# Optimization experiments

Hardware: AMD Instinct MI355X
Metric: run time of the kernel (lower is better)

Reference implementation:

```python
import jax, jax.numpy as jnp
import numpy as np

N_EVENT = 100000
N_TRACE = 20000
E_EE = 1000000
E_ET = 500000
E_TE = 500000
D = 128          # embedding_dim == hidden_dim
OUT = 64         # output_dim
L = 3            # num_layers
NTYPES_EDGES = 3 # edge types
B = 64           # graphs per batch


def setup_inputs() -> dict:
    key = jax.random.key(0)
    ks = jax.random.split(key, 16)
    s = 1.0 / np.sqrt(D)
    inp = {
        "event_ids": jnp.arange(N_EVENT, dtype=jnp.int64 if jax.config.jax_enable_x64 else jnp.int32),
        "trace_ids": jnp.arange(N_TRACE, dtype=jnp.int64 if jax.config.jax_enable_x64 else jnp.int32),
        "e2e_src": jax.random.randint(ks[0], (E_EE,), 0, N_EVENT),
        "e2e_dst": jax.random.randint(ks[1], (E_EE,), 0, N_EVENT),
        "e2t_src": jax.random.randint(ks[2], (E_ET,), 0, N_EVENT),
        "e2t_dst": jax.random.randint(ks[3], (E_ET,), 0, N_TRACE),
        "t2e_src": jax.random.randint(ks[4], (E_TE,), 0, N_TRACE),
        "t2e_dst": jax.random.randint(ks[5], (E_TE,), 0, N_EVENT),
        "event_batch": jnp.sort(jax.random.randint(ks[6], (N_EVENT,), 0, B)),
        "trace_batch": jnp.sort(jax.random.randint(ks[7], (N_TRACE,), 0, B)),
        # learned parameters
        "emb_event": jax.random.normal(ks[8], (N_EVENT, D), jnp.float32),
        "emb_trace": jax.random.normal(ks[9], (N_TRACE, D), jnp.float32),
        # per-layer, per-edge-type SAGEConv weights: lin_l (neighbor, with bias), lin_r (root, no bias)
        "Wl": jax.random.normal(ks[10], (L, NTYPES_EDGES, D, D), jnp.float32) * s,
        "bl": jnp.zeros((L, NTYPES_EDGES, D), jnp.float32),
        "Wr": jax.random.normal(ks[11], (L, NTYPES_EDGES, D, D), jnp.float32) * s,
        # output MLP head
        "W1": jax.random.normal(ks[12], (D, D), jnp.float32) * s,
        "b1": jnp.zeros((D,), jnp.float32),
        "W2": jax.random.normal(ks[13], (OUT, D), jnp.float32) * s,
        "b2": jnp.zeros((OUT,), jnp.float32),
    }
    return inp


def reference(event_ids, trace_ids, e2e_src, e2e_dst, e2t_src, e2t_dst,
              t2e_src, t2e_dst, event_batch, trace_batch,
              emb_event, emb_trace, Wl, bl, Wr, W1, b1, W2, b2):
    def seg_mean(x_src, src, dst, n_dst):
        # mean-aggregate source features onto destination nodes (SAGEConv default aggr)
        s = jax.ops.segment_sum(x_src[src], dst, num_segments=n_dst)
        c = jax.ops.segment_sum(jnp.ones(dst.shape, x_src.dtype), dst, num_segments=n_dst)
        return s / jnp.maximum(c, 1.0)[:, None]

    # per-node-type embedding lookup
    x = {"event": emb_event[event_ids], "trace": emb_trace[trace_ids]}
    n = {"event": event_ids.shape[0], "trace": trace_ids.shape[0]}
    # edge types: (src_type, dst_type, src_idx, dst_idx), conv index matches Wl/bl/Wr axis 1
    edges = [
        ("event", "event", e2e_src, e2e_dst),
        ("event", "trace", e2t_src, e2t_dst),
        ("trace", "event", t2e_src, t2e_dst),
    ]
    n_layers = Wl.shape[0]
    for l in range(n_layers):
        new = {k: jnp.zeros((n[k], Wl.shape[-2]), x[k].dtype) for k in x}
        for i, (st, dt, s_idx, d_idx) in enumerate(edges):
            m = seg_mean(x[st], s_idx, d_idx, n[dt])
            # SAGEConv: lin_l(mean neighbors) + lin_r(root); HeteroConv aggr='sum' across edge types
            new[dt] = new[dt] + m @ Wl[l, i].T + bl[l, i] + x[dt] @ Wr[l, i].T
        x = new
    # global_add_pool per node type, then stack+sum over node types
    pooled = (jax.ops.segment_sum(x["event"], event_batch, num_segments=B)
              + jax.ops.segment_sum(x["trace"], trace_batch, num_segments=B))
    h = jax.nn.relu(pooled @ W1.T + b1)
    return h @ W2.T + b2
```

## Files before the change

kernel.cpp:

```cpp
#include <hip/hip_runtime.h>
#include <hip/hip_bf16.h>


#define D 128
#define NB 64
#define OUTD 64
#define NLAY 3
#define EPB 4096
#define BSH2 9
#define PSPLIT 4

typedef __bf16 bf16;
typedef __bf16 bf16x4 __attribute__((ext_vector_type(4)));
typedef __bf16 bf16x8 __attribute__((ext_vector_type(8)));
typedef float  f32x16 __attribute__((ext_vector_type(16)));

#define LOAD16_TO_LDS(gp, lp) \
    __builtin_amdgcn_global_load_lds((const __attribute__((address_space(1))) void*)(gp), \
                                     (__attribute__((address_space(3))) void*)(lp), 16, 0, 0)

__device__ __forceinline__ void pool_block_dev(const bf16* __restrict__ x, int s,
                                               const int* __restrict__ bounds, int b, int j,
                                               float* __restrict__ pooled5, float red[16][D]) {
    int start = bounds[b], end = bounds[b + 1];
    int len = end - start;
    if (len <= 0) return;
    int r0 = start + (int)(((long long)len * j) / PSPLIT);
    int r1 = start + (int)(((long long)len * (j + 1)) / PSPLIT);
    if (r0 >= r1) return;
    int slot = threadIdx.x >> 4;
    int ch   = threadIdx.x & 15;
    float a[8] = {};
    for (int r = r0 + slot; r < r1; r += 16) {
        bf16x8 v = ((const bf16x8*)(x + (size_t)r * D))[ch];
        #pragma unroll
        for (int e = 0; e < 8; ++e) a[e] += (float)v[e];
    }
    #pragma unroll
    for (int e = 0; e < 8; ++e) red[slot][ch * 8 + e] = a[e];
    __syncthreads();
    int c = threadIdx.x;
    if (c < D) {
        float ssum = 0.f;
        #pragma unroll
        for (int k = 0; k < 16; ++k) ssum += red[k][c];
        atomicAdd(&pooled5[(size_t)s * NB * D + b * D + c], ssum);
    }
}

__global__ void front_all(const float* __restrict__ embE, const int* __restrict__ idsE,
                          bf16* __restrict__ xE, int nE,
                          const float* __restrict__ embT, const int* __restrict__ idsT,
                          bf16* __restrict__ xT, int nT,
                          const int* __restrict__ bEv, const int* __restrict__ bTr,
                          int* __restrict__ boundsE, int* __restrict__ boundsT,
                          const int* __restrict__ dEE, int nEE, int nbkEE, int nblkEE,
                          int* __restrict__ cntEE,
                          const int* __restrict__ dET, int nET, int nbkET, int nblkET,
                          int* __restrict__ cntET,
                          const int* __restrict__ dTE, int nTE, int nbkTE, int nblkTE,
                          int* __restrict__ cntTE,
                          const float* __restrict__ Wl, const float* __restrict__ Wr,
                          const float* __restrict__ bl,
                          bf16* __restrict__ wbuf, float* __restrict__ bbuf,
                          float* __restrict__ pooled5, int nGather) {
    __shared__ int h[256];
    int b = blockIdx.x;
    if (b < nGather) {
        int idx = b * 256 + threadIdx.x;
        const float* emb; const int* ids; bf16* x;
        int tE = nE * 32;
        if (idx < tE) { emb = embE; ids = idsE; x = xE; }
        else {
            idx -= tE;
            if (idx >= nT * 32) return;
            emb = embT; ids = idsT; x = xT;
        }
        int r = idx >> 5, v = idx & 31;
        float4 f = ((const float4*)(emb + (size_t)ids[r] * D))[v];
        bf16x4 o;
        o[0] = (bf16)f.x; o[1] = (bf16)f.y; o[2] = (bf16)f.z; o[3] = (bf16)f.w;
        ((bf16x4*)(x + (size_t)r * D))[v] = o;
        return;
    }
    b -= nGather;
    int nblkH = nblkEE + nblkET + nblkTE;
    if (b < nblkH) {
        const int* dst; int E, nbk, nblk, lb; int* cnt;
        if (b < nblkEE) { dst = dEE; E = nEE; nbk = nbkEE; nblk = nblkEE; cnt = cntEE; lb = b; }
        else if (b < nblkEE + nblkET) { dst = dET; E = nET; nbk = nbkET; nblk = nblkET; cnt = cntET; lb = b - nblkEE; }
        else { dst = dTE; E = nTE; nbk = nbkTE; nblk = nblkTE; cnt = cntTE; lb = b - nblkEE - nblkET; }
        h[threadIdx.x] = 0;
        __syncthreads();
        int e0 = lb * EPB, e1 = min(e0 + EPB, E);
        for (int e = e0 + threadIdx.x; e < e1; e += 256) atomicAdd(&h[dst[e] >> BSH2], 1);
        __syncthreads();
        for (int k = threadIdx.x; k < nbk; k += 256) cnt[k * nblk + lb] = h[k];
        return;
    }
    b -= nblkH;
    if (b < 120) {
        int idx = b * 256 + threadIdx.x;
        if (idx >= NLAY * 5 * 2048) return;
        int l = idx / (5 * 2048);
        int rem = idx - l * 5 * 2048;
        int mat = rem >> 11;
        int q = rem & 2047;
        int lane = q & 63, t = (q >> 6) & 7, w = q >> 9;
        int r = w * 32 + (lane & 31);
        int c = t * 16 + (lane >> 5) * 8;
        size_t l3 = (size_t)l * 3;
        const float* s0;
        const float* s1 = nullptr;
        switch (mat) {
            case 0: s0 = Wl + (l3 + 0) * D * D; break;
            case 1: s0 = Wl + (l3 + 2) * D * D; break;
            case 2: s0 = Wr + (l3 + 0) * D * D; s1 = Wr + (l3 + 2) * D * D; break;
            case 3: s0 = Wl + (l3 + 1) * D * D; break;
            default: s0 = Wr + (l3 + 1) * D * D; break;
        }
        bf16x8 hi, lo;
        #pragma unroll
        for (int e = 0; e < 8; ++e) {
            float v = s0[r * D + c + e];
            if (s1) v += s1[r * D + c + e];
            bf16 hh = (bf16)v;
            hi[e] = hh;
            lo[e] = (bf16)(v - (float)hh);
        }
        bf16* base = wbuf + (size_t)l * 10 * D * D;
        ((bf16x8*)(base + (size_t)(2 * mat) * D * D))[q] = hi;
        ((bf16x8*)(base + (size_t)(2 * mat + 1) * D * D))[q] = lo;
        return;
    }
    b -= 120;
    if (b < 2) {
        int idx = b * 256 + threadIdx.x;
        if (idx >= NLAY * D) return;
        int l = idx >> 7, o = idx & (D - 1);
        bbuf[l * 2 * D + o]     = bl[(size_t)(l * 3 + 0) * D + o] + bl[(size_t)(l * 3 + 2) * D + o];
        bbuf[l * 2 * D + D + o] = bl[(size_t)(l * 3 + 1) * D + o];
        return;
    }
    b -= 2;
    if (b == 0) {
        int t = threadIdx.x;
        if (t <= NB) {
            int lo = 0, hi = nE;
            while (lo < hi) { int mid = (lo + hi) >> 1; if (bEv[mid] < t) lo = mid + 1; else hi = mid; }
            boundsE[t] = lo;
        } else if (t <= 2 * NB + 1) {
            int v = t - NB - 1;
            int lo = 0, hi = nT;
            while (lo < hi) { int mid = (lo + hi) >> 1; if (bTr[mid] < v) lo = mid + 1; else hi = mid; }
            boundsT[v] = lo;
        }
        return;
    }
    b -= 1;
    int idx = b * 256 + threadIdx.x;
    if (idx < 5 * NB * D / 4)
        ((float4*)pooled5)[idx] = make_float4(0.f, 0.f, 0.f, 0.f);
}

__global__ void scan_p1_all(const int* __restrict__ dA, int* __restrict__ oA, int* __restrict__ sA, int nA,
                            const int* __restrict__ dB, int* __restrict__ oB, int* __restrict__ sB, int nB,
                            const int* __restrict__ dC, int* __restrict__ oC, int* __restrict__ sC, int nC) {
    int nbA = (nA + 1023) >> 10, nbB = (nB + 1023) >> 10;
    int b = blockIdx.x;
    const int* deg; int* off; int* bsum; int n; int lb;
    if (b < nbA) { deg = dA; off = oA; bsum = sA; n = nA; lb = b; }
    else if (b < nbA + nbB) { deg = dB; off = oB; bsum = sB; n = nB; lb = b - nbA; }
    else { deg = dC; off = oC; bsum = sC; n = nC; lb = b - nbA - nbB; }
    __shared__ int s[256];
    int t = threadIdx.x;
    int base = lb * 1024 + t * 4;
    int v[4];
    #pragma unroll
    for (int i = 0; i < 4; ++i) v[i] = (base + i < n) ? deg[base + i] : 0;
    int tot = v[0] + v[1] + v[2] + v[3];
    s[t] = tot;
    __syncthreads();
    for (int st = 1; st < 256; st <<= 1) {
        int x = (t >= st) ? s[t - st] : 0;
        __syncthreads();
        s[t] += x;
        __syncthreads();
    }
    int run = s[t] - tot;
    #pragma unroll
    for (int i = 0; i < 4; ++i) {
        if (base + i < n) off[base + i] = run;
        run += v[i];
    }
    if (t == 255) bsum[lb] = s[255];
}

__global__ void scan_p23_all(int* __restrict__ oA, const int* __restrict__ sA, int nA,
                             int* __restrict__ oB, const int* __restrict__ sB, int nB,
                             int* __restrict__ oC, const int* __restrict__ sC, int nC) {
    int cbA = (nA + 255) >> 8, cbB = (nB + 255) >> 8;
    int b = blockIdx.x;
    int* off; const int* bsum; int n; int lb;
    if (b < cbA) { off = oA; bsum = sA; n = nA; lb = b; }
    else if (b < cbA + cbB) { off = oB; bsum = sB; n = nB; lb = b - cbA; }
    else { off = oC; bsum = sC; n = nC; lb = b - cbA - cbB; }
    __shared__ int s[256];
    __shared__ int ex[256];
    int nb = (n + 1023) >> 10;
    int t = threadIdx.x;
    int v = (t < nb) ? bsum[t] : 0;
    s[t] = v;
    __syncthreads();
    for (int st = 1; st < 256; st <<= 1) {
        int x = (t >= st) ? s[t - st] : 0;
        __syncthreads();
        s[t] += x;
        __syncthreads();
    }
    ex[t] = s[t] - v;
    __syncthreads();
    int i = lb * 256 + t;
    if (i < n) off[i] += ex[i >> 10];
    if (i == 0) off[n] = s[nb - 1];
}

__global__ void bkt_scatter_all(const int* __restrict__ sEE, const int* __restrict__ dEE,
                                int nEE, int nbkEE, int nblkEE, const int* __restrict__ SEE,
                                int2* __restrict__ ebEE,
                                const int* __restrict__ sET, const int* __restrict__ dET,
                                int nET, int nbkET, int nblkET, const int* __restrict__ SET,
                                int2* __restrict__ ebET,
                                const int* __restrict__ sTE, const int* __restrict__ dTE,
                                int nTE, int nbkTE, int nblkTE, const int* __restrict__ STE,
                                int2* __restrict__ ebTE) {
    __shared__ int cu[256];
    int b = blockIdx.x;
    const int* src; const int* dst; const int* S; int2* eb; int E, nbk, nblk, lb;
    if (b < nblkEE) { src = sEE; dst = dEE; S = SEE; eb = ebEE; E = nEE; nbk = nbkEE; nblk = nblkEE; lb = b; }
    else if (b < nblkEE + nblkET) { src = sET; dst = dET; S = SET; eb = ebET; E = nET; nbk = nbkET; nblk = nblkET; lb = b - nblkEE; }
    else { src = sTE; dst = dTE; S = STE; eb = ebTE; E = nTE; nbk = nbkTE; nblk = nblkTE; lb = b - nblkEE - nblkET; }
    for (int k = threadIdx.x; k < nbk; k += 256) cu[k] = S[k * nblk + lb];
    __syncthreads();
    int e0 = lb * EPB, e1 = min(e0 + EPB, E);
    for (int e = e0 + threadIdx.x; e < e1; e += 256) {
        int s = src[e], d = dst[e];
        int p = atomicAdd(&cu[d >> BSH2], 1);
        eb[p] = make_int2(s, d);
    }
}

__global__ void csr_build_all(const int2* __restrict__ ebEE, const int* __restrict__ SEE,
                              int nbkEE, int nblkEE, int ndEE,
                              int* __restrict__ offEE, int* __restrict__ adjEE,
                              const int2* __restrict__ ebET, const int* __restrict__ SET,
                              int nbkET, int nblkET, int ndET,
                              int* __restrict__ offET, int* __restrict__ adjET,
                              const int2* __restrict__ ebTE, const int* __restrict__ STE,
                              int nbkTE, int nblkTE, int ndTE,
                              int* __restrict__ offTE, int* __restrict__ adjTE) {
    __shared__ int h[512];
    __shared__ int ps[256];
    __shared__ int cc[512];
    int b = blockIdx.x;
    const int2* eb; const int* S; int nbk, nblk, ndst, k; int* off; int* adj;
    if (b < nbkEE) { eb = ebEE; S = SEE; nbk = nbkEE; nblk = nblkEE; ndst = ndEE; off = offEE; adj = adjEE; k = b; }
    else if (b < nbkEE + nbkET) { eb = ebET; S = SET; nbk = nbkET; nblk = nblkET; ndst = ndET; off = offET; adj = adjET; k = b - nbkEE; }
    else { eb = ebTE; S = STE; nbk = nbkTE; nblk = nblkTE; ndst = ndTE; off = offTE; adj = adjTE; k = b - nbkEE - nbkET; }
    int base = S[k * nblk];
    int end  = (k == nbk - 1) ? S[nbk * nblk] : S[(k + 1) * nblk];
    int d0 = k << BSH2;
    int t = threadIdx.x;
    h[t] = 0; h[t + 256] = 0;
    __syncthreads();
    for (int j = base + t; j < end; j += 256) atomicAdd(&h[eb[j].y - d0], 1);
    __syncthreads();
    int a0 = h[2 * t], a1 = h[2 * t + 1];
    ps[t] = a0 + a1;
    __syncthreads();
    for (int st = 1; st < 256; st <<= 1) {
        int x = (t >= st) ? ps[t - st] : 0;
        __syncthreads();
        ps[t] += x;
        __syncthreads();
    }
    int pe = ps[t] - (a0 + a1);
    int o0 = base + pe, o1 = base + pe + a0;
    cc[2 * t] = o0; cc[2 * t + 1] = o1;
    int nd = min(512, ndst - d0);
    if (2 * t < nd) off[d0 + 2 * t] = o0;
    if (2 * t + 1 < nd) off[d0 + 2 * t + 1] = o1;
    if (t == 0 && k == nbk - 1) off[ndst] = end;
    __syncthreads();
    for (int j = base + t; j < end; j += 256) {
        int2 e = eb[j];
        int p = atomicAdd(&cc[e.y - d0], 1);
        adj[p] = e.x;
    }
}

__global__ void agg_all(const bf16* __restrict__ xE, const bf16* __restrict__ xT,
                        const int* __restrict__ offEE, const int* __restrict__ adjEE,
                        const int* __restrict__ offTE, const int* __restrict__ adjTE,
                        const int* __restrict__ offET, const int* __restrict__ adjET,
                        bf16* __restrict__ mEE, bf16* __restrict__ mTE, bf16* __restrict__ mET,
                        int nE, int nT, int aggBlocks,
                        const int* __restrict__ boundsE, const int* __restrict__ boundsT,
                        float* __restrict__ pooled5) {
    __shared__ float red[16][D];
    if ((int)blockIdx.x >= aggBlocks) {
        int idx = (int)blockIdx.x - aggBlocks;
        int j2 = idx / (NB * PSPLIT);
        int rem = idx - j2 * NB * PSPLIT;
        int bb = rem / PSPLIT, jj = rem - bb * PSPLIT;
        if (j2 == 0) pool_block_dev(xE, 2, boundsE, bb, jj, pooled5, red);
        else         pool_block_dev(xT, 4, boundsT, bb, jj, pooled5, red);
        return;
    }
    int gw = (blockIdx.x * blockDim.x + threadIdx.x) >> 6;
    int lane = threadIdx.x & 63;
    int qE = (nE + 3) >> 2, qT = (nT + 3) >> 2;
    const bf16* xsrc; const int* off; const int* adj; bf16* out; int ndst;
    if (gw < qE) { xsrc = xE; off = offEE; adj = adjEE; out = mEE; ndst = nE; }
    else if (gw < 2 * qE) { gw -= qE; xsrc = xT; off = offTE; adj = adjTE; out = mTE; ndst = nE; }
    else {
        gw -= 2 * qE;
        if (gw >= qT) return;
        xsrc = xE; off = offET; adj = adjET; out = mET; ndst = nT;
    }
    int sub = lane >> 4;
    int sl  = lane & 15;
    int row = gw * 4 + sub;
    if (row >= ndst) row = ndst - 1;
    int s0 = off[row], s1 = off[row + 1];
    float a[8] = {};
    int j = s0;
    for (; j + 8 <= s1; j += 8) {
        int ii[8];
        #pragma unroll
        for (int u = 0; u < 8; ++u) ii[u] = adj[j + u];
        bf16x8 v[8];
        #pragma unroll
        for (int u = 0; u < 8; ++u) v[u] = ((const bf16x8*)(xsrc + (size_t)ii[u] * D))[sl];
        #pragma unroll
        for (int u = 0; u < 8; ++u)
            #pragma unroll
            for (int e = 0; e < 8; ++e) a[e] += (float)v[u][e];
    }
    for (; j + 4 <= s1; j += 4) {
        int i0 = adj[j], i1 = adj[j + 1], i2 = adj[j + 2], i3 = adj[j + 3];
        bf16x8 v0 = ((const bf16x8*)(xsrc + (size_t)i0 * D))[sl];
        bf16x8 v1 = ((const bf16x8*)(xsrc + (size_t)i1 * D))[sl];
        bf16x8 v2 = ((const bf16x8*)(xsrc + (size_t)i2 * D))[sl];
        bf16x8 v3 = ((const bf16x8*)(xsrc + (size_t)i3 * D))[sl];
        #pragma unroll
        for (int e = 0; e < 8; ++e)
            a[e] += (float)v0[e] + (float)v1[e] + (float)v2[e] + (float)v3[e];
    }
    for (; j < s1; ++j) {
        int i0 = adj[j];
        bf16x8 v0 = ((const bf16x8*)(xsrc + (size_t)i0 * D))[sl];
        #pragma unroll
        for (int e = 0; e < 8; ++e) a[e] += (float)v0[e];
    }
    float inv = 1.0f / fmaxf((float)(s1 - s0), 1.0f);
    bf16x8 o;
    #pragma unroll
    for (int e = 0; e < 8; ++e) o[e] = (bf16)(a[e] * inv);
    ((bf16x8*)(out + (size_t)row * D))[sl] = o;
}

__device__ __forceinline__ void gemm_body(const bf16* A0, const bf16* A1, const bf16* A2,
                                          const bf16* Wp, const float* bias, bf16* out,
                                          int M, int nm, int row0, bf16* As) {
    int tid = threadIdx.x;
    int wave = tid >> 6, lane = tid & 63;
    int m = lane & 31, half = lane >> 5;

    f32x16 acc[2];
    #pragma unroll
    for (int rt = 0; rt < 2; ++rt)
        #pragma unroll
        for (int i = 0; i < 16; ++i) acc[rt][i] = 0.f;

    const bf16* Aptr[3] = {A0, A1, A2};
    #pragma unroll
    for (int s = 0; s < 3; ++s) {
        if (s >= nm) break;
        if (s) __syncthreads();
        const bf16* Amat = Aptr[s];
        #pragma unroll
        for (int p = 0; p < 4; ++p) {
            int si = p * 256 + tid;
            int r = si >> 4, u = si & 15;
            int gr = row0 + r; if (gr >= M) gr = M - 1;
            int gc = (u ^ (r & 15)) * 8;
            LOAD16_TO_LDS(Amat + (size_t)gr * D + gc, As + (size_t)(p * 4 + wave) * 512);
        }
        const bf16* wph = Wp + (size_t)(2 * s) * D * D + ((size_t)wave * 512 + lane) * 8;
        const bf16* wpl = wph + D * D;
        bf16x8 bh_c  = *(const bf16x8*)(wph);
        bf16x8 blo_c = *(const bf16x8*)(wpl);
        __syncthreads();

        #pragma unroll 1
        for (int t = 0; t < 8; ++t) {
            bf16x8 bh_n, blo_n;
            if (t < 7) {
                bh_n  = *(const bf16x8*)(wph + (t + 1) * 512);
                blo_n = *(const bf16x8*)(wpl + (t + 1) * 512);
            }
            bf16x8 af[2];
            #pragma unroll
            for (int rt = 0; rt < 2; ++rt) {
                int r = rt * 32 + m;
                int c = t * 2 + half;
                af[rt] = *(const bf16x8*)(As + ((size_t)r * 16 + (c ^ (r & 15))) * 8);
            }
            acc[0] = __builtin_amdgcn_mfma_f32_32x32x16_bf16(af[0], bh_c,  acc[0], 0, 0, 0);
            acc[1] = __builtin_amdgcn_mfma_f32_32x32x16_bf16(af[1], bh_c,  acc[1], 0, 0, 0);
            acc[0] = __builtin_amdgcn_mfma_f32_32x32x16_bf16(af[0], blo_c, acc[0], 0, 0, 0);
            acc[1] = __builtin_amdgcn_mfma_f32_32x32x16_bf16(af[1], blo_c, acc[1], 0, 0, 0);
            bh_c = bh_n; blo_c = blo_n;
        }
    }

    int col = wave * 32 + m;
    float bv = bias[col];
    #pragma unroll
    for (int rt = 0; rt < 2; ++rt) {
        #pragma unroll
        for (int r = 0; r < 16; ++r) {
            int row = row0 + rt * 32 + (r & 3) + 8 * (r >> 2) + 4 * half;
            if (row < M) out[(size_t)row * D + col] = (bf16)(acc[rt][r] + bv);
        }
    }
}

__global__ __launch_bounds__(256) void gemm_all(const bf16* __restrict__ eA0, const bf16* __restrict__ eA1,
                                                const bf16* __restrict__ eA2, const bf16* __restrict__ eW,
                                                const float* __restrict__ eB, bf16* __restrict__ eOut,
                                                int Me, int bE,
                                                const bf16* __restrict__ tA0, const bf16* __restrict__ tA1,
                                                const bf16* __restrict__ tW, const float* __restrict__ tB,
                                                bf16* __restrict__ tOut, int Mt) {
    __shared__ bf16 As[64 * 128];
    if ((int)blockIdx.x < bE)
        gemm_body(eA0, eA1, eA2, eW, eB, eOut, Me, 3, blockIdx.x * 64, As);
    else
        gemm_body(tA0, tA1, (const bf16*)nullptr, tW, tB, tOut, Mt, 2,
                  ((int)blockIdx.x - bE) * 64, As);
}

__global__ void pool_m_all(const bf16* __restrict__ m_ee, const bf16* __restrict__ m_te,
                           const bf16* __restrict__ m_et,
                           const int* __restrict__ boundsE, const int* __restrict__ boundsT,
                           float* __restrict__ pooled5) {
    __shared__ float red[16][D];
    int blk = blockIdx.x;
    int s3 = blk / (NB * PSPLIT);
    int rem = blk - s3 * NB * PSPLIT;
    int b = rem / PSPLIT, j = rem - b * PSPLIT;
    if (s3 == 0)      pool_block_dev(m_ee, 0, boundsE, b, j, pooled5, red);
    else if (s3 == 1) pool_block_dev(m_te, 1, boundsE, b, j, pooled5, red);
    else              pool_block_dev(m_et, 3, boundsT, b, j, pooled5, red);
}

__global__ void tail_kernel(const float* __restrict__ pooled5,
                            const int* __restrict__ boundsE, const int* __restrict__ boundsT,
                            const float* __restrict__ Wl, const float* __restrict__ Wr,
                            const float* __restrict__ bl,
                            const float* __restrict__ W1, const float* __restrict__ b1,
                            const float* __restrict__ W2, const float* __restrict__ b2,
                            float* __restrict__ out) {
    __shared__ float p5[5][D];
    __shared__ float hp[D];
    __shared__ float hh[D];
    int b = blockIdx.x, t = threadIdx.x;
    #pragma unroll
    for (int s = 0; s < 5; ++s) p5[s][t] = pooled5[(size_t)(s * NB + b) * D + t];
    __syncthreads();
    float ce = (float)(boundsE[b + 1] - boundsE[b]);
    float ct = (float)(boundsT[b + 1] - boundsT[b]);
    float s = ce * (bl[6 * D + t] + bl[8 * D + t]) + ct * bl[7 * D + t];
    const float* w0  = Wl + (size_t)6 * D * D + (size_t)t * D;
    const float* w2  = Wl + (size_t)8 * D * D + (size_t)t * D;
    const float* wr0 = Wr + (size_t)6 * D * D + (size_t)t * D;
    const float* wr2 = Wr + (size_t)8 * D * D + (size_t)t * D;
    const float* w1m = Wl + (size_t)7 * D * D + (size_t)t * D;
    const float* wr1 = Wr + (size_t)7 * D * D + (size_t)t * D;
    #pragma unroll 4
    for (int k = 0; k < D; ++k)
        s += p5[0][k] * w0[k] + p5[1][k] * w2[k] + p5[2][k] * (wr0[k] + wr2[k])
           + p5[3][k] * w1m[k] + p5[4][k] * wr1[k];
    hp[t] = s;
    __syncthreads();
    float s1 = b1[t];
    const float* u = W1 + (size_t)t * D;
    #pragma unroll 4
    for (int k = 0; k < D; ++k) s1 += hp[k] * u[k];
    hh[t] = fmaxf(s1, 0.f);
    __syncthreads();
    if (t < OUTD) {
        float s2 = b2[t];
        const float* v = W2 + (size_t)t * D;
        #pragma unroll 4
        for (int k = 0; k < D; ++k) s2 += hh[k] * v[k];
        out[b * OUTD + t] = s2;
    }
}

extern "C" void kernel_launch(void* const* d_in, const int* in_sizes, int n_in,
                              void* d_out, int out_size, void* d_ws, size_t ws_size,
                              hipStream_t stream) {
    const int* event_ids   = (const int*)d_in[0];
    const int* trace_ids   = (const int*)d_in[1];
    const int* e2e_src     = (const int*)d_in[2];
    const int* e2e_dst     = (const int*)d_in[3];
    const int* e2t_src     = (const int*)d_in[4];
    const int* e2t_dst     = (const int*)d_in[5];
    const int* t2e_src     = (const int*)d_in[6];
    const int* t2e_dst     = (const int*)d_in[7];
    const int* event_batch = (const int*)d_in[8];
    const int* trace_batch = (const int*)d_in[9];
    const float* emb_event = (const float*)d_in[10];
    const float* emb_trace = (const float*)d_in[11];
    const float* Wl        = (const float*)d_in[12];
    const float* bl        = (const float*)d_in[13];
    const float* Wr        = (const float*)d_in[14];
    const float* W1        = (const float*)d_in[15];
    const float* b1        = (const float*)d_in[16];
    const float* W2        = (const float*)d_in[17];
    const float* b2        = (const float*)d_in[18];

    const int NE = in_sizes[0];
    const int NT = in_sizes[1];
    const int EE = in_sizes[2];
    const int ET = in_sizes[4];
    const int TE = in_sizes[6];

    const int nbkEE = (NE + 511) >> BSH2, nblkEE = (EE + EPB - 1) / EPB;
    const int nbkET = (NT + 511) >> BSH2, nblkET = (ET + EPB - 1) / EPB;
    const int nbkTE = (NE + 511) >> BSH2, nblkTE = (TE + EPB - 1) / EPB;
    const int cEE = nbkEE * nblkEE, cET = nbkET * nblkET, cTE = nbkTE * nblkTE;

    size_t cur = 0;
    auto alloc = [&](size_t bytes) -> void* {
        cur = (cur + 255) & ~(size_t)255;
        void* p = (char*)d_ws + cur;
        cur += bytes;
        return p;
    };
    bf16* x_event   = (bf16*)alloc((size_t)NE * D * 2);
    bf16* x_trace   = (bf16*)alloc((size_t)NT * D * 2);
    bf16* nx_event  = (bf16*)alloc((size_t)NE * D * 2);
    bf16* nx_trace  = (bf16*)alloc((size_t)NT * D * 2);
    bf16* m_ee      = (bf16*)alloc((size_t)NE * D * 2);
    bf16* m_te      = (bf16*)alloc((size_t)NE * D * 2);
    bf16* m_et      = (bf16*)alloc((size_t)NT * D * 2);
    bf16* wbuf      = (bf16*)alloc((size_t)NLAY * 10 * D * D * 2);
    float* bbuf     = (float*)alloc((size_t)NLAY * 2 * D * 4);
    float* pooled5  = (float*)alloc((size_t)5 * NB * D * 4);
    int* boundsE = (int*)alloc((size_t)(NB + 1) * 4);
    int* boundsT = (int*)alloc((size_t)(NB + 1) * 4);
    int* off_ee = (int*)alloc((size_t)(NE + 1) * 4);
    int* adj_ee = (int*)alloc((size_t)EE * 4);
    int* off_et = (int*)alloc((size_t)(NT + 1) * 4);
    int* adj_et = (int*)alloc((size_t)ET * 4);
    int* off_te = (int*)alloc((size_t)(NE + 1) * 4);
    int* adj_te = (int*)alloc((size_t)TE * 4);
    int* cnt_ee = (int*)alloc((size_t)cEE * 4);
    int* S_ee   = (int*)alloc((size_t)(cEE + 1) * 4);
    int* cnt_et = (int*)alloc((size_t)cET * 4);
    int* S_et   = (int*)alloc((size_t)(cET + 1) * 4);
    int* cnt_te = (int*)alloc((size_t)cTE * 4);
    int* S_te   = (int*)alloc((size_t)(cTE + 1) * 4);
    int* bsum_ee = (int*)alloc(((size_t)(cEE + 1023) / 1024 + 1) * 4);
    int* bsum_et = (int*)alloc(((size_t)(cET + 1023) / 1024 + 1) * 4);
    int* bsum_te = (int*)alloc(((size_t)(cTE + 1023) / 1024 + 1) * 4);
    int2* eb_ee = (int2*)m_ee;
    int2* eb_et = (int2*)m_te;
    int2* eb_te = (int2*)m_et;
    (void)ws_size; (void)n_in; (void)out_size;

    const int nGather = ((NE + NT) * 32 + 255) / 256;
    const int nblkH = nblkEE + nblkET + nblkTE;
    front_all<<<nGather + nblkH + 120 + 2 + 1 + 40, 256, 0, stream>>>(
        emb_event, event_ids, x_event, NE, emb_trace, trace_ids, x_trace, NT,
        event_batch, trace_batch, boundsE, boundsT,
        e2e_dst, EE, nbkEE, nblkEE, cnt_ee,
        e2t_dst, ET, nbkET, nblkET, cnt_et,
        t2e_dst, TE, nbkTE, nblkTE, cnt_te,
        Wl, Wr, bl, wbuf, bbuf, pooled5, nGather);

    const int nb1 = (cEE + 1023) >> 10, nb2 = (cET + 1023) >> 10, nb3 = (cTE + 1023) >> 10;
    scan_p1_all<<<nb1 + nb2 + nb3, 256, 0, stream>>>(
        cnt_ee, S_ee, bsum_ee, cEE, cnt_et, S_et, bsum_et, cET, cnt_te, S_te, bsum_te, cTE);
    scan_p23_all<<<((cEE + 255) >> 8) + ((cET + 255) >> 8) + ((cTE + 255) >> 8), 256, 0, stream>>>(
        S_ee, bsum_ee, cEE, S_et, bsum_et, cET, S_te, bsum_te, cTE);
    bkt_scatter_all<<<nblkEE + nblkET + nblkTE, 256, 0, stream>>>(
        e2e_src, e2e_dst, EE, nbkEE, nblkEE, S_ee, eb_ee,
        e2t_src, e2t_dst, ET, nbkET, nblkET, S_et, eb_et,
        t2e_src, t2e_dst, TE, nbkTE, nblkTE, S_te, eb_te);
    csr_build_all<<<nbkEE + nbkET + nbkTE, 256, 0, stream>>>(
        eb_ee, S_ee, nbkEE, nblkEE, NE, off_ee, adj_ee,
        eb_et, S_et, nbkET, nblkET, NT, off_et, adj_et,
        eb_te, S_te, nbkTE, nblkTE, NE, off_te, adj_te);

    const int qE = (NE + 3) >> 2, qT = (NT + 3) >> 2;
    const int aggBlocks = (2 * qE + qT + 3) / 4;
    const int bE = (NE + 63) / 64, bT = (NT + 63) / 64;
    for (int l = 0; l < NLAY; ++l) {
        int extra = (l == NLAY - 1) ? 2 * NB * PSPLIT : 0;
        agg_all<<<aggBlocks + extra, 256, 0, stream>>>(x_event, x_trace,
                                                       off_ee, adj_ee, off_te, adj_te, off_et, adj_et,
                                                       m_ee, m_te, m_et, NE, NT, aggBlocks,
                                                       boundsE, boundsT, pooled5);
        if (l < NLAY - 1) {
            const bf16* wl_ev = wbuf + (size_t)l * 10 * D * D;
            const bf16* wl_tr = wl_ev + (size_t)6 * D * D;
            const float* be = bbuf + (size_t)l * 2 * D;
            const float* bt = be + D;
            gemm_all<<<bE + bT, 256, 0, stream>>>(m_ee, m_te, x_event, wl_ev, be, nx_event, NE, bE,
                                                  m_et, x_trace, wl_tr, bt, nx_trace, NT);
            bf16* t;
            t = x_event; x_event = nx_event; nx_event = t;
            t = x_trace; x_trace = nx_trace; nx_trace = t;
        }
    }

    pool_m_all<<<3 * NB * PSPLIT, 256, 0, stream>>>(m_ee, m_te, m_et,
                                                    boundsE, boundsT, pooled5);
    tail_kernel<<<NB, D, 0, stream>>>(pooled5, boundsE, boundsT, Wl, Wr, bl,
                                      W1, b1, W2, b2, (float*)d_out);
}
```

Baseline: 561.2 us.

## Merge CSR build phases and pooling tail into cooperative kernels with grid sync

Four CSR construction kernels (scan phase 1, scan phase 2/3, bucket scatter, CSR build) become one cooperative kernel that separates the phases with grid-wide syncs. The pooling and MLP-tail kernels are likewise merged into a second cooperative kernel. The aim is to cut kernel launch overhead and inter-kernel gaps. In exchange, each phase runs on a fixed grid of 512 blocks with grid.sync barriers, which can add barrier cost and reduce parallelism for phases that used more blocks.

```diff
diff --git a/kernel.cpp b/kernel.cpp
--- a/kernel.cpp
+++ b/kernel.cpp
@@ -1,5 +1,8 @@
 #include <hip/hip_runtime.h>
 #include <hip/hip_bf16.h>
+#include <hip/hip_cooperative_groups.h>
+
+namespace cg = cooperative_groups;
 
 
 #define D 128
@@ -9,6 +12,8 @@
 #define EPB 4096
 #define BSH2 9
 #define PSPLIT 4
+#define CSRGRID 512
+#define FINGRID 512
 
 typedef __bf16 bf16;
 typedef __bf16 bf16x4 __attribute__((ext_vector_type(4)));
@@ -46,6 +51,7 @@
         for (int k = 0; k < 16; ++k) ssum += red[k][c];
         atomicAdd(&pooled5[(size_t)s * NB * D + b * D + c], ssum);
     }
+    __syncthreads();
 }
 
 __global__ void front_all(const float* __restrict__ embE, const int* __restrict__ idsE,
@@ -163,16 +169,25 @@
         ((float4*)pooled5)[idx] = make_float4(0.f, 0.f, 0.f, 0.f);
 }
 
-__global__ void scan_p1_all(const int* __restrict__ dA, int* __restrict__ oA, int* __restrict__ sA, int nA,
-                            const int* __restrict__ dB, int* __restrict__ oB, int* __restrict__ sB, int nB,
-                            const int* __restrict__ dC, int* __restrict__ oC, int* __restrict__ sC, int nC) {
-    int nbA = (nA + 1023) >> 10, nbB = (nB + 1023) >> 10;
-    int b = blockIdx.x;
+struct CsrArgs {
+    const int *sEE, *dEE, *sET, *dET, *sTE, *dTE;
+    int nEE, nET, nTE;
+    int nbkEE, nblkEE, nbkET, nblkET, nbkTE, nblkTE;
+    int cEE, cET, cTE;
+    int *cnt_ee, *S_ee, *cnt_et, *S_et, *cnt_te, *S_te;
+    int *bsum_ee, *bsum_et, *bsum_te;
+    int2 *eb_ee, *eb_et, *eb_te;
+    int *off_ee, *adj_ee, *off_et, *adj_et, *off_te, *adj_te;
+    int ndEE, ndET, ndTE;
+};
+
+__device__ void scan_p1_dev(int b, const CsrArgs& A, int* sh) {
+    int nbA = (A.cEE + 1023) >> 10, nbB = (A.cET + 1023) >> 10;
     const int* deg; int* off; int* bsum; int n; int lb;
-    if (b < nbA) { deg = dA; off = oA; bsum = sA; n = nA; lb = b; }
-    else if (b < nbA + nbB) { deg = dB; off = oB; bsum = sB; n = nB; lb = b - nbA; }
-    else { deg = dC; off = oC; bsum = sC; n = nC; lb = b - nbA - nbB; }
-    __shared__ int s[256];
+    if (b < nbA) { deg = A.cnt_ee; off = A.S_ee; bsum = A.bsum_ee; n = A.cEE; lb = b; }
+    else if (b < nbA + nbB) { deg = A.cnt_et; off = A.S_et; bsum = A.bsum_et; n = A.cET; lb = b - nbA; }
+    else { deg = A.cnt_te; off = A.S_te; bsum = A.bsum_te; n = A.cTE; lb = b - nbA - nbB; }
+    int* s = sh;
     int t = threadIdx.x;
     int base = lb * 1024 + t * 4;
     int v[4];
@@ -194,19 +209,17 @@
         run += v[i];
     }
     if (t == 255) bsum[lb] = s[255];
-}
-
-__global__ void scan_p23_all(int* __restrict__ oA, const int* __restrict__ sA, int nA,
-                             int* __restrict__ oB, const int* __restrict__ sB, int nB,
-                             int* __restrict__ oC, const int* __restrict__ sC, int nC) {
-    int cbA = (nA + 255) >> 8, cbB = (nB + 255) >> 8;
-    int b = blockIdx.x;
+    __syncthreads();
+}
+
+__device__ void scan_p23_dev(int b, const CsrArgs& A, int* sh) {
+    int cbA = (A.cEE + 255) >> 8, cbB = (A.cET + 255) >> 8;
     int* off; const int* bsum; int n; int lb;
-    if (b < cbA) { off = oA; bsum = sA; n = nA; lb = b; }
-    else if (b < cbA + cbB) { off = oB; bsum = sB; n = nB; lb = b - cbA; }
-    else { off = oC; bsum = sC; n = nC; lb = b - cbA - cbB; }
-    __shared__ int s[256];
-    __shared__ int ex[256];
+    if (b < cbA) { off = A.S_ee; bsum = A.bsum_ee; n = A.cEE; lb = b; }
+    else if (b < cbA + cbB) { off = A.S_et; bsum = A.bsum_et; n = A.cET; lb = b - cbA; }
+    else { off = A.S_te; bsum = A.bsum_te; n = A.cTE; lb = b - cbA - cbB; }
+    int* s = sh;
+    int* ex = sh + 256;
     int nb = (n + 1023) >> 10;
     int t = threadIdx.x;
     int v = (t < nb) ? bsum[t] : 0;
@@ -223,23 +236,15 @@
     int i = lb * 256 + t;
     if (i < n) off[i] += ex[i >> 10];
     if (i == 0) off[n] = s[nb - 1];
-}
-
-__global__ void bkt_scatter_all(const int* __restrict__ sEE, const int* __restrict__ dEE,
-                                int nEE, int nbkEE, int nblkEE, const int* __restrict__ SEE,
-                                int2* __restrict__ ebEE,
-                                const int* __restrict__ sET, const int* __restrict__ dET,
-                                int nET, int nbkET, int nblkET, const int* __restrict__ SET,
-                                int2* __restrict__ ebET,
-                                const int* __restrict__ sTE, const int* __restrict__ dTE,
-                                int nTE, int nbkTE, int nblkTE, const int* __restrict__ STE,
-                                int2* __restrict__ ebTE) {
-    __shared__ int cu[256];
-    int b = blockIdx.x;
+    __syncthreads();
+}
+
+__device__ void scatter_dev(int b, const CsrArgs& A, int* sh) {
     const int* src; const int* dst; const int* S; int2* eb; int E, nbk, nblk, lb;
-    if (b < nblkEE) { src = sEE; dst = dEE; S = SEE; eb = ebEE; E = nEE; nbk = nbkEE; nblk = nblkEE; lb = b; }
-    else if (b < nblkEE + nblkET) { src = sET; dst = dET; S = SET; eb = ebET; E = nET; nbk = nbkET; nblk = nblkET; lb = b - nblkEE; }
-    else { src = sTE; dst = dTE; S = STE; eb = ebTE; E = nTE; nbk = nbkTE; nblk = nblkTE; lb = b - nblkEE - nblkET; }
+    if (b < A.nblkEE) { src = A.sEE; dst = A.dEE; S = A.S_ee; eb = A.eb_ee; E = A.nEE; nbk = A.nbkEE; nblk = A.nblkEE; lb = b; }
+    else if (b < A.nblkEE + A.nblkET) { src = A.sET; dst = A.dET; S = A.S_et; eb = A.eb_et; E = A.nET; nbk = A.nbkET; nblk = A.nblkET; lb = b - A.nblkEE; }
+    else { src = A.sTE; dst = A.dTE; S = A.S_te; eb = A.eb_te; E = A.nTE; nbk = A.nbkTE; nblk = A.nblkTE; lb = b - A.nblkEE - A.nblkET; }
+    int* cu = sh;
     for (int k = threadIdx.x; k < nbk; k += 256) cu[k] = S[k * nblk + lb];
     __syncthreads();
     int e0 = lb * EPB, e1 = min(e0 + EPB, E);
@@ -248,25 +253,17 @@
         int p = atomicAdd(&cu[d >> BSH2], 1);
         eb[p] = make_int2(s, d);
     }
-}
-
-__global__ void csr_build_all(const int2* __restrict__ ebEE, const int* __restrict__ SEE,
-                              int nbkEE, int nblkEE, int ndEE,
-                              int* __restrict__ offEE, int* __restrict__ adjEE,
-                              const int2* __restrict__ ebET, const int* __restrict__ SET,
-                              int nbkET, int nblkET, int ndET,
-                              int* __restrict__ offET, int* __restrict__ adjET,
-                              const int2* __restrict__ ebTE, const int* __restrict__ STE,
-                              int nbkTE, int nblkTE, int ndTE,
-                              int* __restrict__ offTE, int* __restrict__ adjTE) {
-    __shared__ int h[512];
-    __shared__ int ps[256];
-    __shared__ int cc[512];
-    int b = blockIdx.x;
+    __syncthreads();
+}
+
+__device__ void build_dev(int b, const CsrArgs& A, int* sh) {
     const int2* eb; const int* S; int nbk, nblk, ndst, k; int* off; int* adj;
-    if (b < nbkEE) { eb = ebEE; S = SEE; nbk = nbkEE; nblk = nblkEE; ndst = ndEE; off = offEE; adj = adjEE; k = b; }
-    else if (b < nbkEE + nbkET) { eb = ebET; S = SET; nbk = nbkET; nblk = nblkET; ndst = ndET; off = offET; adj = adjET; k = b - nbkEE; }
-    else { eb = ebTE; S = STE; nbk = nbkTE; nblk = nblkTE; ndst = ndTE; off = offTE; adj = adjTE; k = b - nbkEE - nbkET; }
+    if (b < A.nbkEE) { eb = A.eb_ee; S = A.S_ee; nbk = A.nbkEE; nblk = A.nblkEE; ndst = A.ndEE; off = A.off_ee; adj = A.adj_ee; k = b; }
+    else if (b < A.nbkEE + A.nbkET) { eb = A.eb_et; S = A.S_et; nbk = A.nbkET; nblk = A.nblkET; ndst = A.ndET; off = A.off_et; adj = A.adj_et; k = b - A.nbkEE; }
+    else { eb = A.eb_te; S = A.S_te; nbk = A.nbkTE; nblk = A.nblkTE; ndst = A.ndTE; off = A.off_te; adj = A.adj_te; k = b - A.nbkEE - A.nbkET; }
+    int* h = sh;
+    int* ps = sh + 512;
+    int* cc = sh + 768;
     int base = S[k * nblk];
     int end  = (k == nbk - 1) ? S[nbk * nblk] : S[(k + 1) * nblk];
     int d0 = k << BSH2;
@@ -297,6 +294,24 @@
         int p = atomicAdd(&cc[e.y - d0], 1);
         adj[p] = e.x;
     }
+    __syncthreads();
+}
+
+__global__ void csr_coop(CsrArgs A) {
+    __shared__ int sh[1280];
+    cg::grid_group grid = cg::this_grid();
+    int nb1 = (A.cEE + 1023) >> 10, nb2 = (A.cET + 1023) >> 10, nb3 = (A.cTE + 1023) >> 10;
+    int nScan1 = nb1 + nb2 + nb3;
+    for (int vb = blockIdx.x; vb < nScan1; vb += gridDim.x) scan_p1_dev(vb, A, sh);
+    grid.sync();
+    int nScan23 = ((A.cEE + 255) >> 8) + ((A.cET + 255) >> 8) + ((A.cTE + 255) >> 8);
+    for (int vb = blockIdx.x; vb < nScan23; vb += gridDim.x) scan_p23_dev(vb, A, sh);
+    grid.sync();
+    int nScat = A.nblkEE + A.nblkET + A.nblkTE;
+    for (int vb = blockIdx.x; vb < nScat; vb += gridDim.x) scatter_dev(vb, A, sh);
+    grid.sync();
+    int nBld = A.nbkEE + A.nbkET + A.nbkTE;
+    for (int vb = blockIdx.x; vb < nBld; vb += gridDim.x) build_dev(vb, A, sh);
 }
 
 __global__ void agg_all(const bf16* __restrict__ xE, const bf16* __restrict__ xT,
@@ -452,61 +467,68 @@
                   ((int)blockIdx.x - bE) * 64, As);
 }
 
-__global__ void pool_m_all(const bf16* __restrict__ m_ee, const bf16* __restrict__ m_te,
-                           const bf16* __restrict__ m_et,
-                           const int* __restrict__ boundsE, const int* __restrict__ boundsT,
-                           float* __restrict__ pooled5) {
+struct FinArgs {
+    const bf16 *m_ee, *m_te, *m_et;
+    const int *boundsE, *boundsT;
+    float* pooled5;
+    const float *Wl, *Wr, *bl, *W1, *b1, *W2, *b2;
+    float* out;
+};
+
+__global__ void finish_coop(FinArgs A) {
     __shared__ float red[16][D];
-    int blk = blockIdx.x;
-    int s3 = blk / (NB * PSPLIT);
-    int rem = blk - s3 * NB * PSPLIT;
-    int b = rem / PSPLIT, j = rem - b * PSPLIT;
-    if (s3 == 0)      pool_block_dev(m_ee, 0, boundsE, b, j, pooled5, red);
-    else if (s3 == 1) pool_block_dev(m_te, 1, boundsE, b, j, pooled5, red);
-    else              pool_block_dev(m_et, 3, boundsT, b, j, pooled5, red);
-}
-
-__global__ void tail_kernel(const float* __restrict__ pooled5,
-                            const int* __restrict__ boundsE, const int* __restrict__ boundsT,
-                            const float* __restrict__ Wl, const float* __restrict__ Wr,
-                            const float* __restrict__ bl,
-                            const float* __restrict__ W1, const float* __restrict__ b1,
-                            const float* __restrict__ W2, const float* __restrict__ b2,
-                            float* __restrict__ out) {
-    __shared__ float p5[5][D];
-    __shared__ float hp[D];
-    __shared__ float hh[D];
+    cg::grid_group grid = cg::this_grid();
+    for (int vb = blockIdx.x; vb < 3 * NB * PSPLIT; vb += gridDim.x) {
+        int s3 = vb / (NB * PSPLIT);
+        int rem = vb - s3 * NB * PSPLIT;
+        int b = rem / PSPLIT, j = rem - b * PSPLIT;
+        if (s3 == 0)      pool_block_dev(A.m_ee, 0, A.boundsE, b, j, A.pooled5, red);
+        else if (s3 == 1) pool_block_dev(A.m_te, 1, A.boundsE, b, j, A.pooled5, red);
+        else              pool_block_dev(A.m_et, 3, A.boundsT, b, j, A.pooled5, red);
+    }
+    grid.sync();
+    if ((int)blockIdx.x >= NB) return;
+    float* p5 = &red[0][0];
+    float* hp = p5 + 5 * D;
+    float* hh = hp + D;
     int b = blockIdx.x, t = threadIdx.x;
-    #pragma unroll
-    for (int s = 0; s < 5; ++s) p5[s][t] = pooled5[(size_t)(s * NB + b) * D + t];
-    __syncthreads();
-    float ce = (float)(boundsE[b + 1] - boundsE[b]);
-    float ct = (float)(boundsT[b + 1] - boundsT[b]);
-    float s = ce * (bl[6 * D + t] + bl[8 * D + t]) + ct * bl[7 * D + t];
-    const float* w0  = Wl + (size_t)6 * D * D + (size_t)t * D;
-    const float* w2  = Wl + (size_t)8 * D * D + (size_t)t * D;
-    const float* wr0 = Wr + (size_t)6 * D * D + (size_t)t * D;
-    const float* wr2 = Wr + (size_t)8 * D * D + (size_t)t * D;
-    const float* w1m = Wl + (size_t)7 * D * D + (size_t)t * D;
-    const float* wr1 = Wr + (size_t)7 * D * D + (size_t)t * D;
-    #pragma unroll 4
-    for (int k = 0; k < D; ++k)
-        s += p5[0][k] * w0[k] + p5[1][k] * w2[k] + p5[2][k] * (wr0[k] + wr2[k])
-           + p5[3][k] * w1m[k] + p5[4][k] * wr1[k];
-    hp[t] = s;
-    __syncthreads();
-    float s1 = b1[t];
-    const float* u = W1 + (size_t)t * D;
-    #pragma unroll 4
-    for (int k = 0; k < D; ++k) s1 += hp[k] * u[k];
-    hh[t] = fmaxf(s1, 0.f);
+    if (t < D) {
+        #pragma unroll
+        for (int s = 0; s < 5; ++s) p5[s * D + t] = A.pooled5[(size_t)(s * NB + b) * D + t];
+    }
+    __syncthreads();
+    const float* Wl = A.Wl; const float* Wr = A.Wr; const float* bl = A.bl;
+    if (t < D) {
+        float ce = (float)(A.boundsE[b + 1] - A.boundsE[b]);
+        float ct = (float)(A.boundsT[b + 1] - A.boundsT[b]);
+        float s = ce * (bl[6 * D + t] + bl[8 * D + t]) + ct * bl[7 * D + t];
+        const float* w0  = Wl + (size_t)6 * D * D + (size_t)t * D;
+        const float* w2  = Wl + (size_t)8 * D * D + (size_t)t * D;
+        const float* wr0 = Wr + (size_t)6 * D * D + (size_t)t * D;
+        const float* wr2 = Wr + (size_t)8 * D * D + (size_t)t * D;
+        const float* w1m = Wl + (size_t)7 * D * D + (size_t)t * D;
+        const float* wr1 = Wr + (size_t)7 * D * D + (size_t)t * D;
+        #pragma unroll 4
+        for (int k = 0; k < D; ++k)
+            s += p5[0 * D + k] * w0[k] + p5[1 * D + k] * w2[k] + p5[2 * D + k] * (wr0[k] + wr2[k])
+               + p5[3 * D + k] * w1m[k] + p5[4 * D + k] * wr1[k];
+        hp[t] = s;
+    }
+    __syncthreads();
+    if (t < D) {
+        float s1 = A.b1[t];
+        const float* u = A.W1 + (size_t)t * D;
+        #pragma unroll 4
+        for (int k = 0; k < D; ++k) s1 += hp[k] * u[k];
+        hh[t] = fmaxf(s1, 0.f);
+    }
     __syncthreads();
     if (t < OUTD) {
-        float s2 = b2[t];
-        const float* v = W2 + (size_t)t * D;
+        float s2 = A.b2[t];
+        const float* v = A.W2 + (size_t)t * D;
         #pragma unroll 4
         for (int k = 0; k < D; ++k) s2 += hh[k] * v[k];
-        out[b * OUTD + t] = s2;
+        A.out[b * OUTD + t] = s2;
     }
 }
 
@@ -593,19 +615,24 @@
         t2e_dst, TE, nbkTE, nblkTE, cnt_te,
         Wl, Wr, bl, wbuf, bbuf, pooled5, nGather);
 
-    const int nb1 = (cEE + 1023) >> 10, nb2 = (cET + 1023) >> 10, nb3 = (cTE + 1023) >> 10;
-    scan_p1_all<<<nb1 + nb2 + nb3, 256, 0, stream>>>(
-        cnt_ee, S_ee, bsum_ee, cEE, cnt_et, S_et, bsum_et, cET, cnt_te, S_te, bsum_te, cTE);
-    scan_p23_all<<<((cEE + 255) >> 8) + ((cET + 255) >> 8) + ((cTE + 255) >> 8), 256, 0, stream>>>(
-        S_ee, bsum_ee, cEE, S_et, bsum_et, cET, S_te, bsum_te, cTE);
-    bkt_scatter_all<<<nblkEE + nblkET + nblkTE, 256, 0, stream>>>(
-        e2e_src, e2e_dst, EE, nbkEE, nblkEE, S_ee, eb_ee,
-        e2t_src, e2t_dst, ET, nbkET, nblkET, S_et, eb_et,
-        t2e_src, t2e_dst, TE, nbkTE, nblkTE, S_te, eb_te);
-    csr_build_all<<<nbkEE + nbkET + nbkTE, 256, 0, stream>>>(
-        eb_ee, S_ee, nbkEE, nblkEE, NE, off_ee, adj_ee,
-        eb_et, S_et, nbkET, nblkET, NT, off_et, adj_et,
-        eb_te, S_te, nbkTE, nblkTE, NE, off_te, adj_te);
+    CsrArgs ca;
+    ca.sEE = e2e_src; ca.dEE = e2e_dst; ca.sET = e2t_src; ca.dET = e2t_dst;
+    ca.sTE = t2e_src; ca.dTE = t2e_dst;
+    ca.nEE = EE; ca.nET = ET; ca.nTE = TE;
+    ca.nbkEE = nbkEE; ca.nblkEE = nblkEE; ca.nbkET = nbkET; ca.nblkET = nblkET;
+    ca.nbkTE = nbkTE; ca.nblkTE = nblkTE;
+    ca.cEE = cEE; ca.cET = cET; ca.cTE = cTE;
+    ca.cnt_ee = cnt_ee; ca.S_ee = S_ee; ca.cnt_et = cnt_et; ca.S_et = S_et;
+    ca.cnt_te = cnt_te; ca.S_te = S_te;
+    ca.bsum_ee = bsum_ee; ca.bsum_et = bsum_et; ca.bsum_te = bsum_te;
+    ca.eb_ee = eb_ee; ca.eb_et = eb_et; ca.eb_te = eb_te;
+    ca.off_ee = off_ee; ca.adj_ee = adj_ee; ca.off_et = off_et; ca.adj_et = adj_et;
+    ca.off_te = off_te; ca.adj_te = adj_te;
+    ca.ndEE = NE; ca.ndET = NT; ca.ndTE = NE;
+    {
+        void* kp[] = { &ca };
+        hipLaunchCooperativeKernel((void*)csr_coop, dim3(CSRGRID), dim3(256), kp, 0, stream);
+    }
 
     const int qE = (NE + 3) >> 2, qT = (NT + 3) >> 2;
     const int aggBlocks = (2 * qE + qT + 3) / 4;
@@ -629,8 +656,15 @@
         }
     }
 
-    pool_m_all<<<3 * NB * PSPLIT, 256, 0, stream>>>(m_ee, m_te, m_et,
-                                                    boundsE, boundsT, pooled5);
-    tail_kernel<<<NB, D, 0, stream>>>(pooled5, boundsE, boundsT, Wl, Wr, bl,
-                                      W1, b1, W2, b2, (float*)d_out);
-}
+    FinArgs fa;
+    fa.m_ee = m_ee; fa.m_te = m_te; fa.m_et = m_et;
+    fa.boundsE = boundsE; fa.boundsT = boundsT;
+    fa.pooled5 = pooled5;
+    fa.Wl = Wl; fa.Wr = Wr; fa.bl = bl;
+    fa.W1 = W1; fa.b1 = b1; fa.W2 = W2; fa.b2 = b2;
+    fa.out = (float*)d_out;
+    {
+        void* kp[] = { &fa };
+        hipLaunchCooperativeKernel((void*)finish_coop, dim3(FINGRID), dim3(256), kp, 0, stream);
+    }
+}
```

Result: slower. 837.4 us (+49.2%).
